# Kernel tuning notes

Measured on AMD Instinct MI355X. Metric: run time of the kernel, lower is better.

Reference implementation:

```python
import jax, jax.numpy as jnp
import numpy as np

D_MODEL = 1024

def setup_inputs() -> dict:
    key = jax.random.key(0)
    k1, k2 = jax.random.split(key, 2)
    x = jax.random.normal(k1, (4, 2048, D_MODEL), dtype=jnp.float32)
    W_attn = jax.random.normal(k2, (3 * D_MODEL, D_MODEL), dtype=jnp.float32) * (1.0 / np.sqrt(D_MODEL))
    b_attn = jnp.zeros((3 * D_MODEL,), dtype=jnp.float32)
    return {"x": x, "W_attn": W_attn, "b_attn": b_attn}

def reference(x, W_attn, b_attn):
    B, T, C = x.shape
    # fused QKV projection; torch split order is (k, q, v)
    kqv = x @ W_attn.T + b_attn            # [B, T, 3C]
    k, q, v = jnp.split(kqv, 3, axis=-1)   # each [B, T, C]
    # NOTE: original computes k @ q^T (quirk), scaled by sqrt(d_model)
    scores = jnp.einsum('btc,bsc->bts', k, q) / jnp.sqrt(jnp.asarray(C, x.dtype))
    causal = jnp.tril(jnp.ones((T, T), dtype=bool))
    scores = jnp.where(causal[None, :, :], scores, -jnp.inf)
    attn = jax.nn.softmax(scores, axis=-1)
    return jnp.einsum('bts,bsc->btc', attn, v)
```

## Files before the change

### kernel.cpp

```cpp
#include <hip/hip_runtime.h>

typedef __bf16 bf16x8 __attribute__((ext_vector_type(8)));
typedef float f32x4 __attribute__((ext_vector_type(4)));
typedef float fl4 __attribute__((ext_vector_type(4)));
typedef unsigned short us4 __attribute__((ext_vector_type(4)));
typedef unsigned short us8 __attribute__((ext_vector_type(8)));

__device__ __forceinline__ unsigned short f2bf(float f) {
  unsigned u = __builtin_bit_cast(unsigned, f);
  u += 0x7fffu + ((u >> 16) & 1u);
  return (unsigned short)(u >> 16);
}
__device__ __forceinline__ float bf2f(unsigned short h) {
  unsigned u = ((unsigned)h) << 16;
  return __builtin_bit_cast(float, u);
}

__device__ __forceinline__ void async16(const void* g, void* l) {
  __builtin_amdgcn_global_load_lds(
      (const __attribute__((address_space(1))) unsigned int*)g,
      (__attribute__((address_space(3))) unsigned int*)l, 16, 0, 0);
}

#define BARM() asm volatile("s_barrier" ::: "memory")
#define VMCNT4() asm volatile("s_waitcnt vmcnt(4)" ::: "memory")

__global__ __launch_bounds__(256) void cvt_bf16(const float* __restrict__ s,
                                                unsigned short* __restrict__ d, int n4) {
  int i = blockIdx.x * 256 + threadIdx.x;
  if (i >= n4) return;
  fl4 f = ((const fl4*)s)[i];
  us4 o;
  o[0] = f2bf(f[0]); o[1] = f2bf(f[1]); o[2] = f2bf(f[2]); o[3] = f2bf(f[3]);
  ((us4*)d)[i] = o;
}

__global__ __launch_bounds__(256) void transpose_v(const unsigned short* __restrict__ kqv,
                                                   unsigned short* __restrict__ vT) {
  int b = blockIdx.z;
  int t0 = blockIdx.x * 64;
  int c0 = blockIdx.y * 64;
  __shared__ unsigned short tile[64][68];
  int tid = threadIdx.x;
#pragma unroll
  for (int i = 0; i < 4; ++i) {
    int idx = i * 256 + tid;
    int r = idx >> 4;
    int c4 = (idx & 15) * 4;
    const unsigned short* src = kqv + ((size_t)(b * 2048 + t0 + r)) * 3072 + 2048 + c0 + c4;
    us4 v = *(const us4*)src;
    *(us4*)&tile[r][c4] = v;
  }
  __syncthreads();
#pragma unroll
  for (int i = 0; i < 4; ++i) {
    int idx = i * 256 + tid;
    int rc = idx >> 4;
    int t4 = (idx & 15) * 4;
    us4 v;
    v[0] = tile[t4 + 0][rc]; v[1] = tile[t4 + 1][rc];
    v[2] = tile[t4 + 2][rc]; v[3] = tile[t4 + 3][rc];
    unsigned short* dst = vT + ((size_t)(b * 1024 + c0 + rc)) * 2048 + t0 + t4;
    *(us4*)dst = v;
  }
}


template <int EPI>
__global__ __launch_bounds__(512, 2) void gemm8p(
    const unsigned short* __restrict__ A, int lda, long long sA,
    const unsigned short* __restrict__ B, int ldb, long long sB,
    void* __restrict__ Cv, int ldc, long long sC,
    const float* __restrict__ bias, float scale, int K, int NBX) {
  int bx, by;
  const int bz = blockIdx.z;
  if (EPI == 0) {
    int flat = blockIdx.x;
    int q = (int)gridDim.x >> 3;
    int swz = (flat & 7) * q + (flat >> 3);
    bx = swz % NBX; by = swz / NBX;
  } else {
    bx = blockIdx.x; by = blockIdx.y;
    if (EPI == 1 && bx > by) return;
  }
  A += (size_t)bz * sA;
  B += (size_t)bz * sB;
  const int rowBase = by * 256;
  const int colBase = bx * 256;
  const int nk = (EPI == 2) ? (rowBase + 256) / 64 : K / 64;

  __shared__ __align__(16) unsigned char lds[131072];
  const int tid = threadIdx.x;
  const int lane = tid & 63;
  const int wid = tid >> 6;
  const int wr = wid >> 2;
  const int wc = wid & 3;
  const int l15 = lane & 15, l4 = lane >> 4, l7 = lane & 7;

  f32x4 acc[8][4] = {};
  bf16x8 bfr[4][2];

  auto STAGE = [&](int bufc, int isB, int half, const unsigned short* G, int ld,
                   int rbase, int koff) {
#pragma unroll
    for (int i = 0; i < 2; ++i) {
      int off = (i * 512 + tid) * 16;
      int r = off >> 7;
      int sb = ((off >> 4) & 7) ^ (r & 7);
      async16(G + (size_t)(rbase + half * 128 + r) * ld + koff + sb * 8,
              lds + bufc * 65536 + isB * 32768 + half * 16384 + off);
    }
  };
  auto RDA = [&](int bufc, int m, int kk) -> bf16x8 {
    int row = m * 16 + l15;
    int blk = (kk * 4 + l4) ^ l7;
    return *(const bf16x8*)(lds + bufc * 65536 + wr * 16384 + row * 128 + blk * 16);
  };
  auto RDB = [&](int bufc, int n, int kk) -> bf16x8 {
    int row = (wc & 1) * 64 + n * 16 + l15;
    int blk = (kk * 4 + l4) ^ l7;
    return *(const bf16x8*)(lds + bufc * 65536 + 32768 + (wc >> 1) * 16384 +
                            row * 128 + blk * 16);
  };

#define PHASE(BUFC, Q, STAGE_STMT, GATE_STMT)                                  \
  do {                                                                         \
    bf16x8 af[2][2];                                                           \
    if ((Q) == 0) {                                                            \
      _Pragma("unroll") for (int n = 0; n < 4; ++n)                            \
      _Pragma("unroll") for (int kk = 0; kk < 2; ++kk)                         \
          bfr[n][kk] = RDB((BUFC), n, kk);                                     \
    }                                                                          \
    _Pragma("unroll") for (int mi = 0; mi < 2; ++mi)                           \
    _Pragma("unroll") for (int kk = 0; kk < 2; ++kk)                           \
        af[mi][kk] = RDA((BUFC), (Q) * 2 + mi, kk);                            \
    STAGE_STMT;                                                                \
    BARM();                                                                    \
    __builtin_amdgcn_s_setprio(1);                                             \
    _Pragma("unroll") for (int kk = 0; kk < 2; ++kk)                           \
    _Pragma("unroll") for (int mi = 0; mi < 2; ++mi)                           \
    _Pragma("unroll") for (int n = 0; n < 4; ++n)                              \
        acc[(Q) * 2 + mi][n] = __builtin_amdgcn_mfma_f32_16x16x32_bf16(        \
            af[mi][kk], bfr[n][kk], acc[(Q) * 2 + mi][n], 0, 0, 0);            \
    __builtin_amdgcn_s_setprio(0);                                             \
    GATE_STMT;                                                                 \
    BARM();                                                                    \
  } while (0)

  STAGE(0, 0, 0, A, lda, rowBase, 0);
  STAGE(0, 0, 1, A, lda, rowBase, 0);
  STAGE(0, 1, 0, B, ldb, colBase, 0);
  STAGE(0, 1, 1, B, ldb, colBase, 0);
  {
    int k1 = ((1 < nk - 1) ? 1 : (nk - 1)) * 64;
    STAGE(1, 1, 0, B, ldb, colBase, k1);
    STAGE(1, 1, 1, B, ldb, colBase, k1);
  }
  VMCNT4();
  BARM();

  const int nt2 = nk >> 1;
  for (int it = 0; it < nt2; ++it) {
    int t = it * 2;
    int tA1 = t + 1 < nk - 1 ? t + 1 : nk - 1;
    int t2 = t + 2 < nk - 1 ? t + 2 : nk - 1;
    int t3 = t + 3 < nk - 1 ? t + 3 : nk - 1;
    int kA1 = tA1 * 64, k2 = t2 * 64, k3 = t3 * 64;
    PHASE(0, 0, STAGE(1, 0, 0, A, lda, rowBase, kA1), (void)0);
    PHASE(0, 1, STAGE(1, 0, 1, A, lda, rowBase, kA1), (void)0);
    PHASE(0, 2, STAGE(0, 1, 0, B, ldb, colBase, k2), (void)0);
    PHASE(0, 3, STAGE(0, 1, 1, B, ldb, colBase, k2), VMCNT4());
    PHASE(1, 0, STAGE(0, 0, 0, A, lda, rowBase, k2), (void)0);
    PHASE(1, 1, STAGE(0, 0, 1, A, lda, rowBase, k2), (void)0);
    PHASE(1, 2, STAGE(1, 1, 0, B, ldb, colBase, k3), (void)0);
    PHASE(1, 3, STAGE(1, 1, 1, B, ldb, colBase, k3), VMCNT4());
  }
#undef PHASE

  const int cr = l4 * 4;
  if constexpr (EPI == 0) {
    unsigned short* C = (unsigned short*)Cv;
#pragma unroll
    for (int n = 0; n < 4; ++n) {
      int col = colBase + wc * 64 + n * 16 + l15;
      float bv = bias[col];
#pragma unroll
      for (int m = 0; m < 8; ++m) {
        int row = rowBase + wr * 128 + m * 16 + cr;
#pragma unroll
        for (int i = 0; i < 4; ++i)
          C[(size_t)(row + i) * ldc + col] = f2bf(acc[m][n][i] + bv);
      }
    }
  } else if constexpr (EPI == 1) {
    unsigned short* C = (unsigned short*)Cv + (size_t)bz * sC;
#pragma unroll
    for (int n = 0; n < 4; ++n) {
      int col = colBase + wc * 64 + n * 16 + l15;
#pragma unroll
      for (int m = 0; m < 8; ++m) {
        int row = rowBase + wr * 128 + m * 16 + cr;
#pragma unroll
        for (int i = 0; i < 4; ++i)
          C[(size_t)(row + i) * ldc + col] = f2bf(acc[m][n][i] * scale);
      }
    }
  } else {
    float* C = (float*)Cv + (size_t)bz * sC;
#pragma unroll
    for (int n = 0; n < 4; ++n) {
      int col = colBase + wc * 64 + n * 16 + l15;
#pragma unroll
      for (int m = 0; m < 8; ++m) {
        int row = rowBase + wr * 128 + m * 16 + cr;
#pragma unroll
        for (int i = 0; i < 4; ++i)
          C[(size_t)(row + i) * ldc + col] = acc[m][n][i];
      }
    }
  }
}

__global__ __launch_bounds__(256) void softmax_causal(unsigned short* __restrict__ S) {
  const int T = 2048;
  int t = blockIdx.x, b = blockIdx.y;
  unsigned short* row = S + ((size_t)b * T + t) * T;
  const int nv = t + 1;
  int tid = threadIdx.x;
  int lane = tid & 63, wid = tid >> 6;
  int s0 = tid * 8;
  us8 raw = *(const us8*)(row + s0);
  float v[8];
  float m = -3.0e38f;
#pragma unroll
  for (int j = 0; j < 8; ++j) {
    v[j] = bf2f(raw[j]);
    if (s0 + j < nv) m = fmaxf(m, v[j]);
  }
#pragma unroll
  for (int o = 32; o > 0; o >>= 1) m = fmaxf(m, __shfl_xor(m, o, 64));
  __shared__ float red[4];
  if (lane == 0) red[wid] = m;
  __syncthreads();
  m = fmaxf(fmaxf(red[0], red[1]), fmaxf(red[2], red[3]));
  __syncthreads();
  float sum = 0.f;
#pragma unroll
  for (int j = 0; j < 8; ++j) {
    float e = (s0 + j < nv) ? exp2f(v[j] - m) : 0.f;
    v[j] = e;
    sum += e;
  }
#pragma unroll
  for (int o = 32; o > 0; o >>= 1) sum += __shfl_xor(sum, o, 64);
  if (lane == 0) red[wid] = sum;
  __syncthreads();
  sum = red[0] + red[1] + red[2] + red[3];
  float inv = 1.0f / sum;
  us8 outv;
#pragma unroll
  for (int j = 0; j < 8; ++j) outv[j] = f2bf(v[j] * inv);
  *(us8*)(row + s0) = outv;
}

extern "C" void kernel_launch(void* const* d_in, const int* in_sizes, int n_in,
                              void* d_out, int out_size, void* d_ws, size_t ws_size,
                              hipStream_t stream) {
  const float* x = (const float*)d_in[0];
  const float* W = (const float*)d_in[1];
  const float* bias = (const float*)d_in[2];
  float* out = (float*)d_out;

  char* ws = (char*)d_ws;
  if (ws_size < 106954752u) return;
  unsigned short* xbf = (unsigned short*)(ws);
  unsigned short* vT = xbf;
  unsigned short* wbf = (unsigned short*)(ws + 16777216);
  unsigned short* kqv = (unsigned short*)(ws + 23068672);
  unsigned short* S = (unsigned short*)(ws + 73400320);

  const float kSoftmaxScale = 1.4426950408889634f / 32.0f;

  cvt_bf16<<<8192, 256, 0, stream>>>(x, xbf, 2097152);
  cvt_bf16<<<3072, 256, 0, stream>>>(W, wbf, 786432);

  gemm8p<0><<<dim3(384, 1, 1), 512, 0, stream>>>(
      xbf, 1024, 0LL, wbf, 1024, 0LL, kqv, 3072, 0LL, bias, 1.0f, 1024, 12);

  transpose_v<<<dim3(32, 16, 4), 256, 0, stream>>>(kqv, vT);

  gemm8p<1><<<dim3(8, 8, 4), 512, 0, stream>>>(
      kqv, 3072, 2048LL * 3072, kqv + 1024, 3072, 2048LL * 3072,
      S, 2048, 2048LL * 2048, nullptr, kSoftmaxScale, 1024, 0);

  softmax_causal<<<dim3(2048, 4), 256, 0, stream>>>(S);

  gemm8p<2><<<dim3(4, 8, 4), 512, 0, stream>>>(
      S, 2048, 2048LL * 2048, vT, 2048, 1024LL * 2048,
      out, 1024, 2048LL * 1024, nullptr, 1.0f, 2048, 0);
}
```

Baseline: 192.4 us.

## Software-pipeline LDS fragment reads one phase ahead in GEMM main loop

Rebuilds the GEMM phase schedule so each phase issues the LDS reads for the next phase's A/B fragments before running its MFMAs. It uses double-buffered register fragments (af0/af1, bf0/bf1) and does 4x4 MFMA blocks over one k-slice instead of 2x4 over two. Global-to-LDS staging addresses are also precomputed once per thread, which removes per-stage address arithmetic. The goal is to hide LDS read latency behind matrix math. In exchange it uses more registers and adds an lgkmcnt(0) wait per phase. It also moves the vmcnt wait after the barrier, which may weaken cross-wave visibility of the staged tiles.

```diff
diff --git a/kernel.cpp b/kernel.cpp
--- a/kernel.cpp
+++ b/kernel.cpp
@@ -24,6 +24,7 @@
 
 #define BARM() asm volatile("s_barrier" ::: "memory")
 #define VMCNT4() asm volatile("s_waitcnt vmcnt(4)" ::: "memory")
+#define LGKM0() asm volatile("s_waitcnt lgkmcnt(0)" ::: "memory")
 
 __global__ __launch_bounds__(256) void cvt_bf16(const float* __restrict__ s,
                                                 unsigned short* __restrict__ d, int n4) {
@@ -64,7 +65,6 @@
     *(us4*)dst = v;
   }
 }
-
 
 template <int EPI>
 __global__ __launch_bounds__(512, 2) void gemm8p(
@@ -98,18 +98,28 @@
   const int l15 = lane & 15, l4 = lane >> 4, l7 = lane & 7;
 
   f32x4 acc[8][4] = {};
-  bf16x8 bfr[4][2];
-
-  auto STAGE = [&](int bufc, int isB, int half, const unsigned short* G, int ld,
-                   int rbase, int koff) {
-#pragma unroll
-    for (int i = 0; i < 2; ++i) {
-      int off = (i * 512 + tid) * 16;
-      int r = off >> 7;
-      int sb = ((off >> 4) & 7) ^ (r & 7);
-      async16(G + (size_t)(rbase + half * 128 + r) * ld + koff + sb * 8,
-              lds + bufc * 65536 + isB * 32768 + half * 16384 + off);
-    }
+  bf16x8 af0[4], af1[4], bf0[4], bf1[4];
+
+  const unsigned short* Ab = A + (size_t)rowBase * lda;
+  const unsigned short* Bb = B + (size_t)colBase * ldb;
+  unsigned loff[2][2];
+  unsigned lldso[2];
+#pragma unroll
+  for (int i = 0; i < 2; ++i) {
+    int off = (i * 512 + tid) * 16;
+    int r = off >> 7;
+    int sb = ((off >> 4) & 7) ^ (r & 7);
+    lldso[i] = (unsigned)off;
+#pragma unroll
+    for (int h = 0; h < 2; ++h)
+      loff[h][i] = (unsigned)((h * 128 + r) * lda + sb * 8);
+  }
+
+  auto STAGE = [&](int bufc, int isB, int half, const unsigned short* Gb, int koff) {
+#pragma unroll
+    for (int i = 0; i < 2; ++i)
+      async16(Gb + (size_t)(loff[half][i] + (unsigned)koff),
+              lds + bufc * 65536 + isB * 32768 + half * 16384 + lldso[i]);
   };
   auto RDA = [&](int bufc, int m, int kk) -> bf16x8 {
     int row = m * 16 + l15;
@@ -123,42 +133,42 @@
                             row * 128 + blk * 16);
   };
 
-#define PHASE(BUFC, Q, STAGE_STMT, GATE_STMT)                                  \
+#define RDAF(dst, BUF, MB, KK)                                                 \
+  _Pragma("unroll") for (int mi = 0; mi < 4; ++mi) dst[mi] = RDA((BUF), (MB) + mi, (KK))
+#define RDBF2(dst, BUF, N0, KK)                                                \
+  do { dst[N0] = RDB((BUF), (N0), (KK)); dst[(N0) + 1] = RDB((BUF), (N0) + 1, (KK)); } while (0)
+#define RDBF4(dst, BUF, KK)                                                    \
+  _Pragma("unroll") for (int n = 0; n < 4; ++n) dst[n] = RDB((BUF), n, (KK))
+
+#define PH(MB, AFU, BFU, STG, GATE, RDS)                                       \
   do {                                                                         \
-    bf16x8 af[2][2];                                                           \
-    if ((Q) == 0) {                                                            \
-      _Pragma("unroll") for (int n = 0; n < 4; ++n)                            \
-      _Pragma("unroll") for (int kk = 0; kk < 2; ++kk)                         \
-          bfr[n][kk] = RDB((BUFC), n, kk);                                     \
-    }                                                                          \
-    _Pragma("unroll") for (int mi = 0; mi < 2; ++mi)                           \
-    _Pragma("unroll") for (int kk = 0; kk < 2; ++kk)                           \
-        af[mi][kk] = RDA((BUFC), (Q) * 2 + mi, kk);                            \
-    STAGE_STMT;                                                                \
+    STG;                                                                       \
     BARM();                                                                    \
+    GATE;                                                                      \
+    RDS;                                                                       \
     __builtin_amdgcn_s_setprio(1);                                             \
-    _Pragma("unroll") for (int kk = 0; kk < 2; ++kk)                           \
-    _Pragma("unroll") for (int mi = 0; mi < 2; ++mi)                           \
+    _Pragma("unroll") for (int mi = 0; mi < 4; ++mi)                           \
     _Pragma("unroll") for (int n = 0; n < 4; ++n)                              \
-        acc[(Q) * 2 + mi][n] = __builtin_amdgcn_mfma_f32_16x16x32_bf16(        \
-            af[mi][kk], bfr[n][kk], acc[(Q) * 2 + mi][n], 0, 0, 0);            \
+        acc[(MB) + mi][n] = __builtin_amdgcn_mfma_f32_16x16x32_bf16(           \
+            AFU[mi], BFU[n], acc[(MB) + mi][n], 0, 0, 0);                      \
     __builtin_amdgcn_s_setprio(0);                                             \
-    GATE_STMT;                                                                 \
+    LGKM0();                                                                   \
     BARM();                                                                    \
   } while (0)
 
-  STAGE(0, 0, 0, A, lda, rowBase, 0);
-  STAGE(0, 0, 1, A, lda, rowBase, 0);
-  STAGE(0, 1, 0, B, ldb, colBase, 0);
-  STAGE(0, 1, 1, B, ldb, colBase, 0);
+  STAGE(0, 0, 0, Ab, 0);
+  STAGE(0, 0, 1, Ab, 0);
+  STAGE(0, 1, 0, Bb, 0);
+  STAGE(0, 1, 1, Bb, 0);
   {
     int k1 = ((1 < nk - 1) ? 1 : (nk - 1)) * 64;
-    STAGE(1, 1, 0, B, ldb, colBase, k1);
-    STAGE(1, 1, 1, B, ldb, colBase, k1);
+    STAGE(1, 1, 0, Bb, k1);
+    STAGE(1, 1, 1, Bb, k1);
   }
   VMCNT4();
   BARM();
-
+  RDAF(af0, 0, 0, 0);
+  RDBF4(bf0, 0, 0);
   const int nt2 = nk >> 1;
   for (int it = 0; it < nt2; ++it) {
     int t = it * 2;
@@ -166,16 +176,27 @@
     int t2 = t + 2 < nk - 1 ? t + 2 : nk - 1;
     int t3 = t + 3 < nk - 1 ? t + 3 : nk - 1;
     int kA1 = tA1 * 64, k2 = t2 * 64, k3 = t3 * 64;
-    PHASE(0, 0, STAGE(1, 0, 0, A, lda, rowBase, kA1), (void)0);
-    PHASE(0, 1, STAGE(1, 0, 1, A, lda, rowBase, kA1), (void)0);
-    PHASE(0, 2, STAGE(0, 1, 0, B, ldb, colBase, k2), (void)0);
-    PHASE(0, 3, STAGE(0, 1, 1, B, ldb, colBase, k2), VMCNT4());
-    PHASE(1, 0, STAGE(0, 0, 0, A, lda, rowBase, k2), (void)0);
-    PHASE(1, 1, STAGE(0, 0, 1, A, lda, rowBase, k2), (void)0);
-    PHASE(1, 2, STAGE(1, 1, 0, B, ldb, colBase, k3), (void)0);
-    PHASE(1, 3, STAGE(1, 1, 1, B, ldb, colBase, k3), VMCNT4());
-  }
-#undef PHASE
+    PH(0, af0, bf0, STAGE(1, 0, 0, Ab, kA1), (void)0,
+       { RDAF(af1, 0, 4, 0); RDBF2(bf1, 0, 0, 1); });
+    PH(4, af1, bf0, STAGE(1, 0, 1, Ab, kA1), (void)0,
+       { RDAF(af0, 0, 0, 1); RDBF2(bf1, 0, 2, 1); });
+    PH(0, af0, bf1, STAGE(0, 1, 0, Bb, k2), (void)0,
+       { RDAF(af1, 0, 4, 1); });
+    PH(4, af1, bf1, STAGE(0, 1, 1, Bb, k2), VMCNT4(),
+       { RDAF(af0, 1, 0, 0); RDBF4(bf0, 1, 0); });
+    PH(0, af0, bf0, STAGE(0, 0, 0, Ab, k2), (void)0,
+       { RDAF(af1, 1, 4, 0); RDBF2(bf1, 1, 0, 1); });
+    PH(4, af1, bf0, STAGE(0, 0, 1, Ab, k2), (void)0,
+       { RDAF(af0, 1, 0, 1); RDBF2(bf1, 1, 2, 1); });
+    PH(0, af0, bf1, STAGE(1, 1, 0, Bb, k3), (void)0,
+       { RDAF(af1, 1, 4, 1); });
+    PH(4, af1, bf1, STAGE(1, 1, 1, Bb, k3), VMCNT4(),
+       { RDAF(af0, 0, 0, 0); RDBF4(bf0, 0, 0); });
+  }
+#undef PH
+#undef RDAF
+#undef RDBF2
+#undef RDBF4
 
   const int cr = l4 * 4;
   if constexpr (EPI == 0) {
```

Result: no change. 189.7 us (-1.4%).
